# Optimization experiments

Hardware: AMD Instinct MI355X
Metric: run time of the kernel (lower is better)

The kernel has to match this reference:

```python
import jax, jax.numpy as jnp
import numpy as np

G1, G2, G3 = 4.0, 5.0, 10.0   # cfg.SMOOTH.GAMMA1/2/3 (DAMSM defaults)
T_MOCO = 0.05
EPS = 1e-8


def _ce(logits, labels):
    # mean cross-entropy, labels are int class indices
    lp = jax.nn.log_softmax(logits, axis=-1)
    return -jnp.mean(jnp.take_along_axis(lp, labels[:, None], axis=1)[:, 0])


def _norm(x):
    return jnp.sqrt(jnp.sum(x * x, axis=-1, keepdims=True))


def setup_inputs() -> dict:
    key = jax.random.key(0)
    ks = jax.random.split(key, 8)
    B, T, NEF, H, K = 64, 32, 256, 17, 16384
    return {
        "cnn_code": jax.random.normal(ks[0], (B, NEF), jnp.float32),
        "rnn_code": jax.random.normal(ks[1], (B, NEF), jnp.float32),
        "img_features": jax.random.normal(ks[2], (B, NEF, H, H), jnp.float32),
        "words_emb": jax.random.normal(ks[3], (B, T, NEF), jnp.float32),
        "cnn_code_aug": jax.random.normal(ks[4], (B, NEF), jnp.float32),
        "rnn_code_aug": jax.random.normal(ks[5], (B, NEF), jnp.float32),
        "queue": jax.random.normal(ks[6], (NEF, K), jnp.float32),
        "queue_im": jax.random.normal(ks[7], (NEF, K), jnp.float32),
        "sentence_mask": jnp.ones((B, T), jnp.int32),
        "labels": jnp.arange(B, dtype=jnp.int32),
    }


def reference(cnn_code, rnn_code, img_features, words_emb, cnn_code_aug,
              rnn_code_aug, queue, queue_im, sentence_mask, labels):
    B = words_emb.shape[0]
    # ---------- local word-region attention loss (vectorized over the
    # per-sample python loop; sentence_mask is all-ones -> full length) ----------
    q = jnp.transpose(words_emb, (0, 2, 1))                   # [B, nef, T]
    ctx = img_features.reshape(B, img_features.shape[1], -1)  # [B, nef, S]
    # func_attention: scores[i,j,s,t] between query sample i and image j
    scores = jnp.einsum('jcs,ict->ijst', ctx, q)
    attn = jax.nn.softmax(scores, axis=3)        # softmax over words (queryL)
    attn = jax.nn.softmax(G1 * attn, axis=2)     # softmax over regions (sourceL)
    wC = jnp.einsum('jcs,ijst->ijct', ctx, attn)  # weighted context [i,j,nef,T]
    num = jnp.einsum('ict,ijct->ijt', q, wC)
    qn = jnp.sqrt(jnp.sum(q * q, axis=1))[:, None, :]         # [B,1,T]
    wn = jnp.sqrt(jnp.sum(wC * wC, axis=2))                   # [B,B,T]
    cos = num / jnp.clip(qn * wn, EPS, None)                  # [i,j,T]
    sim = jax.nn.logsumexp(G2 * cos, axis=2)                  # log(sum exp(G2*cos))
    S = sim.T * G3                                            # [j, i] as in original cat(dim=1)
    w_loss0 = _ce(S, labels)
    w_loss1 = _ce(S.T, labels)
    # ---------- global contrastive loss ----------
    cn = cnn_code / jnp.clip(_norm(cnn_code), EPS, None)
    rn = rnn_code / jnp.clip(_norm(rnn_code), EPS, None)
    can = cnn_code_aug / jnp.clip(_norm(cnn_code_aug), EPS, None)
    ran = rnn_code_aug / jnp.clip(_norm(rnn_code_aug), EPS, None)
    qz = jax.lax.stop_gradient(queue)
    qzi = jax.lax.stop_gradient(queue_im)
    zeros = jnp.zeros((B,), dtype=labels.dtype)
    log_it = jnp.concatenate([jnp.sum(cn * ran, -1, keepdims=True), cn @ qz], -1) / T_MOCO
    log_ti = jnp.concatenate([jnp.sum(rn * can, -1, keepdims=True), rn @ qzi], -1) / T_MOCO
    m_loss = (_ce(log_it, zeros) + _ce(log_ti, zeros)) / 2.0
    s0 = G3 * (cn @ rn.T)    # cosine(cnn, rnn) * GAMMA3
    s2 = G3 * (rn @ ran.T)   # cosine(rnn, rnn_aug) * GAMMA3
    loss0 = _ce(s0, labels)
    loss1 = _ce(s0.T, labels)
    loss2 = _ce(s2, labels)
    loss3 = _ce(s2.T, labels)
    return jnp.stack([w_loss0, w_loss1, loss0, loss1, m_loss, loss2, loss3])
```

## Files before the change

kernel.cpp:

```cpp
#include <hip/hip_runtime.h>
#include <hip/hip_bf16.h>
#include <math.h>

#define BB   64
#define TT   32
#define CC   256
#define KK   16384
#define G1c  4.0f
#define G2c  5.0f
#define G3c  10.0f
#define INV_T 20.0f
#define EPSF 1e-8f

#define WS_SIM 0
#define WS_S0  4096
#define WS_S2  8192
#define WS_CN  12288
#define WS_RN  28672
#define WS_CAN 45056
#define WS_RAN 61440
#define WS_QN  77824
#define WS_PM  79872
#define WS_PS  (WS_PM + 16384)
#define WS_CNT  (WS_PS + 16384)
#define WS_RNT  (WS_CNT + 16384)
#define WS_CANT (WS_RNT + 16384)
#define WS_RANT (WS_CANT + 16384)
#define WS_F32_TOTAL (WS_RANT + 16384)

#define CTXT_ELEMS (64*320*256)
#define WQ_ELEMS   (64*32*256)
#define WQ_OFF     CTXT_ELEMS
#define CNRN_OFF   (CTXT_ELEMS + WQ_ELEMS)

#define SC_STR 260

typedef __attribute__((ext_vector_type(8))) short short8;
typedef __attribute__((ext_vector_type(4))) short short4v;
typedef __attribute__((ext_vector_type(4))) float float4v;

__device__ __forceinline__ float4v mfma_bf16(short8 a, short8 b, float4v c) {
    return __builtin_amdgcn_mfma_f32_16x16x32_bf16(a, b, c, 0, 0, 0);
}

__device__ __forceinline__ short f2bf(float f) {
    union { float f; unsigned u; } x; x.f = f;
    unsigned r = x.u + 0x7FFFu + ((x.u >> 16) & 1u);
    return (short)(r >> 16);
}

__device__ __forceinline__ short8 ld8(const short* p) {
    short4v lo = *(const short4v*)p;
    short4v hi = *(const short4v*)(p + 4);
    short8 r = {lo[0],lo[1],lo[2],lo[3],hi[0],hi[1],hi[2],hi[3]};
    return r;
}

__global__ __launch_bounds__(256) void prep_kernel(
    const float* __restrict__ cnn, const float* __restrict__ rnn,
    const float* __restrict__ img, const float* __restrict__ wemb,
    const float* __restrict__ cnnA, const float* __restrict__ rnnA,
    float* __restrict__ W)
{
    int bid = blockIdx.x, tid = threadIdx.x;
    short* B16 = (short*)(W + WS_F32_TOTAL);
    short* ctxT = B16;
    short* wq   = B16 + WQ_OFF;
    short* cnrn = B16 + CNRN_OFF;

    if (bid < 256) {
        int mat = bid >> 6, row = bid & 63;
        const float* src = (mat==0)? cnn : (mat==1)? rnn : (mat==2)? cnnA : rnnA;
        float* dst  = W + ((mat==0)? WS_CN  : (mat==1)? WS_RN  : (mat==2)? WS_CAN  : WS_RAN);
        float* dstT = W + ((mat==0)? WS_CNT : (mat==1)? WS_RNT : (mat==2)? WS_CANT : WS_RANT);
        float v = src[row*256 + tid];
        float ss = v*v;
        for (int o=1;o<64;o<<=1) ss += __shfl_xor(ss,o);
        __shared__ float sc[4];
        if ((tid&63)==0) sc[tid>>6] = ss;
        __syncthreads();
        float tot = sc[0]+sc[1]+sc[2]+sc[3];
        float inv = 1.0f / fmaxf(sqrtf(tot), EPSF);
        float nv = v*inv;
        dst[row*256+tid] = nv;
        dstT[tid*64+row] = nv;
        if (mat < 2) cnrn[(mat*64+row)*256 + tid] = f2bf(nv);
    } else if (bid < 320) {
        int i = bid - 256;
        int t = tid >> 3, k = tid & 7;
        const float* wp = wemb + (i*32 + t)*256 + k*32;
        float ss = 0.f;
        for (int c=0;c<32;c++){ float v = wp[c]; ss += v*v; }
        ss += __shfl_xor(ss,1); ss += __shfl_xor(ss,2); ss += __shfl_xor(ss,4);
        if (k==0) W[WS_QN + i*32 + t] = sqrtf(ss);
    } else if (bid < 1600) {
        int b3 = bid - 320; int j = b3 / 20, mt = b3 % 20, s0 = mt*16;
        __shared__ float tile[16*257];
        for (int idx = tid; idx < 4096; idx += 256) {
            int c = idx >> 4, sl = idx & 15, s = s0 + sl;
            float v = (s < 289) ? img[((size_t)(j*256 + c))*289 + s] : 0.0f;
            tile[sl*257 + c] = v;
        }
        __syncthreads();
        for (int idx = tid; idx < 4096; idx += 256) {
            int orr = idx >> 8, c = idx & 255;
            ctxT[((size_t)(j*320 + s0 + orr))*256 + c] = f2bf(tile[orr*257 + c]);
        }
    } else {
        for (int idx = (bid-1600)*256 + tid; idx < WQ_ELEMS; idx += 64*256) {
            wq[idx] = f2bf(wemb[idx]);
        }
    }
}

__global__ __launch_bounds__(256, 2) void attn_moco_kernel(
    const float* __restrict__ queue, const float* __restrict__ queueIm,
    float* __restrict__ W)
{
    __shared__ short ctx_sc[32*SC_STR];
    __shared__ short eTile[2][2][32][36];
    __shared__ float Dp[4][32], Np[4][32];
    __shared__ float wn2P[4][2][2][16];
    __shared__ float redm[4][64], reds[4][64];
    __shared__ float sa0[256], sa1[256];
    __shared__ float part[2][64][4];

    int bid = blockIdx.x, tid = threadIdx.x;
    int lane = tid & 63, wave = tid >> 6;
    int lo16 = lane & 15, quad = lane >> 4;

    const short* B16 = (const short*)(W + WS_F32_TOTAL);

    if (bid >= 320) {
        const short* ctxT = B16;
        const short* wq   = B16 + WQ_OFF;

        int abid = bid - 320;
        int j = abid >> 5, ip = abid & 31;
        int i_l = wave >> 1, mt = wave & 1;
        int i_g = ip*2 + i_l;

        short8 bq[2][8];
        {
            const short* p = wq + i_g*8192;
            #pragma unroll
            for (int nt2=0;nt2<2;nt2++)
                #pragma unroll
                for (int kk=0;kk<8;kk++)
                    bq[nt2][kk] = *(const short8*)(p + (nt2*16+lo16)*256 + kk*32 + quad*8);
        }

        float4v wacc[4][4];
        #pragma unroll
        for (int cm=0;cm<4;cm++)
            #pragma unroll
            for (int cb=0;cb<4;cb++) wacc[cm][cb] = (float4v){0.f,0.f,0.f,0.f};
        float D0=0.f, D1=0.f, N0=0.f, N1=0.f;

        const short* ctxTj = ctxT + (size_t)j * (320*256);
        int s_row = tid >> 3, c0s = (tid & 7)*32;
        int srow_base = mt*16 + quad*4;

        short8 pf[4];
        {
            const short* g = ctxTj + s_row*256 + c0s;
            #pragma unroll
            for (int m=0;m<4;m++) pf[m] = *(const short8*)(g + m*8);
        }

        for (int tile = 0; tile < 10; tile++) {
            {
                short* d = ctx_sc + s_row*SC_STR + c0s;
                #pragma unroll
                for (int k=0;k<8;k++) {
                    short4v w = { pf[k>>1][(k&1)*4+0], pf[k>>1][(k&1)*4+1],
                                  pf[k>>1][(k&1)*4+2], pf[k>>1][(k&1)*4+3] };
                    *(short4v*)(d + k*4) = w;
                }
            }
            __syncthreads();
            if (tile < 9) {
                const short* g = ctxTj + ((tile+1)*32 + s_row)*256 + c0s;
                #pragma unroll
                for (int m=0;m<4;m++) pf[m] = *(const short8*)(g + m*8);
            }

            float4v a0 = {0.f,0.f,0.f,0.f}, a1 = {0.f,0.f,0.f,0.f};
            {
                const short* ar = ctx_sc + (mt*16 + lo16)*SC_STR + quad*8;
                #pragma unroll
                for (int kk=0;kk<8;kk++) {
                    short8 a = ld8(ar + kk*32);
                    a0 = mfma_bf16(a, bq[0][kk], a0);
                    a1 = mfma_bf16(a, bq[1][kk], a1);
                }
            }

            short8 wa[4];
            #pragma unroll
            for (int cm=0;cm<4;cm++) {
                const short* col = ctx_sc + quad*8*SC_STR + wave*64 + cm*16 + lo16;
                short8 v;
                #pragma unroll
                for (int jj=0;jj<8;jj++) v[jj] = col[jj*SC_STR];
                wa[cm] = v;
            }

            int eb = tile & 1;
            #pragma unroll
            for (int r=0;r<4;r++) {
                float mx = fmaxf(a0[r], a1[r]);
                mx = fmaxf(mx, __shfl_xor(mx,1));
                mx = fmaxf(mx, __shfl_xor(mx,2));
                mx = fmaxf(mx, __shfl_xor(mx,4));
                mx = fmaxf(mx, __shfl_xor(mx,8));
                float e0 = __expf(a0[r]-mx), e1 = __expf(a1[r]-mx);
                float z = e0 + e1;
                z += __shfl_xor(z,1); z += __shfl_xor(z,2);
                z += __shfl_xor(z,4); z += __shfl_xor(z,8);
                float rinv = 1.0f/z;
                int s_local = srow_base + r;
                int sg = tile*32 + s_local;
                float ev0 = 0.f, ev1 = 0.f;
                if (sg < 289) {
                    ev0 = __expf(G1c*e0*rinv);
                    ev1 = __expf(G1c*e1*rinv);
                    D0 += ev0; N0 += ev0*a0[r];
                    D1 += ev1; N1 += ev1*a1[r];
                }
                eTile[eb][i_l][lo16][s_local]    = f2bf(ev0);
                eTile[eb][i_l][16+lo16][s_local] = f2bf(ev1);
            }
            __syncthreads();
            {
                short8 bf0 = ld8(&eTile[eb][0][lo16][quad*8]);
                short8 bf1 = ld8(&eTile[eb][0][16+lo16][quad*8]);
                short8 bf2 = ld8(&eTile[eb][1][lo16][quad*8]);
                short8 bf3 = ld8(&eTile[eb][1][16+lo16][quad*8]);
                #pragma unroll
                for (int cm=0;cm<4;cm++) {
                    wacc[cm][0] = mfma_bf16(wa[cm], bf0, wacc[cm][0]);
                    wacc[cm][1] = mfma_bf16(wa[cm], bf1, wacc[cm][1]);
                    wacc[cm][2] = mfma_bf16(wa[cm], bf2, wacc[cm][2]);
                    wacc[cm][3] = mfma_bf16(wa[cm], bf3, wacc[cm][3]);
                }
            }
        }

        D0 += __shfl_xor(D0,16); D0 += __shfl_xor(D0,32);
        D1 += __shfl_xor(D1,16); D1 += __shfl_xor(D1,32);
        N0 += __shfl_xor(N0,16); N0 += __shfl_xor(N0,32);
        N1 += __shfl_xor(N1,16); N1 += __shfl_xor(N1,32);
        if (lane < 16) {
            Dp[wave][lane] = D0; Dp[wave][16+lane] = D1;
            Np[wave][lane] = N0; Np[wave][16+lane] = N1;
        }
        #pragma unroll
        for (int cb=0;cb<4;cb++) {
            float ss = 0.f;
            #pragma unroll
            for (int cm=0;cm<4;cm++)
                #pragma unroll
                for (int r=0;r<4;r++){ float v = wacc[cm][cb][r]; ss += v*v; }
            ss += __shfl_xor(ss,16);
            ss += __shfl_xor(ss,32);
            if (quad==0) wn2P[wave][cb>>1][cb&1][lo16] = ss;
        }
        __syncthreads();

        if (tid < 64) {
            int i_f = tid >> 5, t = tid & 31;
            int nt2 = t >> 4, lo = t & 15;
            float w2 = wn2P[0][i_f][nt2][lo] + wn2P[1][i_f][nt2][lo]
                     + wn2P[2][i_f][nt2][lo] + wn2P[3][i_f][nt2][lo];
            float D = Dp[i_f*2][t] + Dp[i_f*2+1][t];
            float N = Np[i_f*2][t] + Np[i_f*2+1][t];
            int i_gf = ip*2 + i_f;
            float qv = W[WS_QN + i_gf*32 + t];
            float numS = N/D;
            float wnS = sqrtf(w2)/D;
            float v = G2c * (numS / fmaxf(qv*wnS, EPSF));
            float mx = v;
            for (int o=1;o<32;o<<=1) mx = fmaxf(mx, __shfl_xor(mx,o));
            float e = __expf(v-mx);
            for (int o=1;o<32;o<<=1) e += __shfl_xor(e,o);
            if (t==0) W[WS_SIM + i_gf*64 + j] = mx + __logf(e);
        }
    } else if (bid < 256) {
        int mu = bid >> 7, ch = bid & 127;
        const float* Q = mu ? queueIm : queue;
        const short* Abf = B16 + CNRN_OFF + mu*16384;

        short8 afr[4][8];
        #pragma unroll
        for (int mt=0;mt<4;mt++)
            #pragma unroll
            for (int kk=0;kk<8;kk++)
                afr[mt][kk] = *(const short8*)(Abf + (mt*16+lo16)*256 + kk*32 + quad*8);

        float m16[16], s16[16];
        #pragma unroll
        for (int u=0;u<16;u++){ m16[u] = -1e30f; s16[u] = 0.f; }

        for (int t4 = 0; t4 < 2; t4++) {
            int colb = ch*128 + (wave*2 + t4)*16;
            float4v acc[4];
            #pragma unroll
            for (int mt=0;mt<4;mt++) acc[mt] = (float4v){0.f,0.f,0.f,0.f};
            for (int ks = 0; ks < 8; ks++) {
                short8 bfr;
                #pragma unroll
                for (int jj=0;jj<8;jj++) {
                    float bv = Q[(size_t)(ks*32 + quad*8 + jj)*KK + colb + lo16];
                    bfr[jj] = f2bf(bv);
                }
                #pragma unroll
                for (int mt=0;mt<4;mt++) acc[mt] = mfma_bf16(afr[mt][ks], bfr, acc[mt]);
            }
            #pragma unroll
            for (int mt=0;mt<4;mt++)
                #pragma unroll
                for (int r=0;r<4;r++) {
                    float v = acc[mt][r]*INV_T;
                    int u = mt*4+r;
                    float nm = fmaxf(m16[u], v);
                    s16[u] = s16[u]*__expf(m16[u]-nm) + __expf(v-nm);
                    m16[u] = nm;
                }
        }
        #pragma unroll
        for (int u=0;u<16;u++) {
            #pragma unroll
            for (int o=1;o<16;o<<=1) {
                float om = __shfl_xor(m16[u],o), os = __shfl_xor(s16[u],o);
                float nm = fmaxf(m16[u],om);
                s16[u] = s16[u]*__expf(m16[u]-nm) + os*__expf(om-nm);
                m16[u] = nm;
            }
        }
        if (lo16 == 0) {
            #pragma unroll
            for (int u=0;u<16;u++) {
                int row = (u>>2)*16 + quad*4 + (u&3);
                redm[wave][row] = m16[u]; reds[wave][row] = s16[u];
            }
        }
        __syncthreads();
        if (tid < 64) {
            float m = redm[0][tid], s = reds[0][tid];
            for (int w=1;w<4;w++) {
                float om = redm[w][tid], os = reds[w][tid];
                float nm = fmaxf(m,om);
                s = s*__expf(m-nm) + os*__expf(om-nm);
                m = nm;
            }
            W[WS_PM + mu*8192 + ch*64 + tid] = m;
            W[WS_PS + mu*8192 + ch*64 + tid] = s;
        }
    } else {
        int i = bid - 256;
        sa0[tid] = W[WS_CN + i*256 + tid];
        sa1[tid] = W[WS_RN + i*256 + tid];
        __syncthreads();
        const float* B0 = W + WS_RN;
        const float* B1v = W + WS_RAN;
        float av0 = sa0[tid], av1 = sa1[tid];
        for (int jj = 0; jj < 64; jj++) {
            float v0 = av0 * B0[jj*256 + tid];
            float v1 = av1 * B1v[jj*256 + tid];
            for (int o=1;o<64;o<<=1){ v0 += __shfl_xor(v0,o); v1 += __shfl_xor(v1,o); }
            if (lane==0){ part[0][jj][wave]=v0; part[1][jj][wave]=v1; }
        }
        __syncthreads();
        if (tid < 128) {
            int mat = tid>>6, jj = tid&63;
            float s = part[mat][jj][0]+part[mat][jj][1]+part[mat][jj][2]+part[mat][jj][3];
            W[(mat? WS_S2 : WS_S0) + i*64 + jj] = G3c * s;
        }
    }
}

__global__ __launch_bounds__(256) void final_kernel(
    const int* __restrict__ labels, float* __restrict__ W, float* __restrict__ out)
{
    int tid = threadIdx.x;
    __shared__ float mats[3][64][65];
    __shared__ float mmL[2][4][64], ssL[2][4][64];
    __shared__ float cearr[6][64];
    __shared__ float cemoco[128];

    for (int idx = tid; idx < 3*4096; idx += 256) {
        int t = idx >> 12, rem = idx & 4095;
        const float* src = W + (t==0 ? WS_SIM : (t==1 ? WS_S0 : WS_S2));
        mats[t][rem>>6][rem&63] = src[rem];
    }

    {
        int g = tid >> 6, r = tid & 63;
        for (int mu=0; mu<2; mu++) {
            float m = -1e30f, s = 0.f;
            for (int k=0; k<32; k++) {
                int ch = g*32 + k;
                float om = W[WS_PM + mu*8192 + ch*64 + r];
                float os = W[WS_PS + mu*8192 + ch*64 + r];
                float nm = fmaxf(m, om);
                s = s*__expf(m-nm) + os*__expf(om-nm);
                m = nm;
            }
            mmL[mu][g][r] = m; ssL[mu][g][r] = s;
        }
    }
    __syncthreads();

    if (tid < 128) {
        int mu = tid>>6, r = tid&63;
        float m = mmL[mu][0][r], s = ssL[mu][0][r];
        for (int g=1; g<4; g++) {
            float om = mmL[mu][g][r], os = ssL[mu][g][r];
            float nm = fmaxf(m, om);
            s = s*__expf(m-nm) + os*__expf(om-nm);
            m = nm;
        }
        const float* AT = W + (mu ? WS_RNT : WS_CNT);
        const float* BT = W + (mu ? WS_CANT : WS_RANT);
        float dot = 0.f;
        for (int c=0; c<256; c++) dot += AT[c*64 + r]*BT[c*64 + r];
        float v0 = dot*INV_T;
        float nm = fmaxf(m, v0);
        float S = s*__expf(m-nm) + __expf(v0-nm);
        cemoco[tid] = nm + __logf(S) - v0;
    }

    for (int pass=0; pass<2; pass++) {
        int cfg = pass*4 + (tid>>6);
        int row = tid&63;
        if (cfg < 6) {
            int mi; float scale; int colMajor;
            if (cfg==0){ mi=0; scale=G3c; colMajor=1; }
            else if (cfg==1){ mi=0; scale=G3c; colMajor=0; }
            else if (cfg==2){ mi=1; scale=1.f; colMajor=0; }
            else if (cfg==3){ mi=1; scale=1.f; colMajor=1; }
            else if (cfg==4){ mi=2; scale=1.f; colMajor=0; }
            else            { mi=2; scale=1.f; colMajor=1; }
            float mx = -1e30f;
            for (int x=0;x<64;x++) {
                float v = (colMajor? mats[mi][x][row] : mats[mi][row][x])*scale;
                mx = fmaxf(mx, v);
            }
            float se = 0.f;
            for (int x=0;x<64;x++) {
                float v = (colMajor? mats[mi][x][row] : mats[mi][row][x])*scale;
                se += __expf(v-mx);
            }
            int lbl = labels[row];
            float diag = (colMajor? mats[mi][lbl][row] : mats[mi][row][lbl])*scale;
            cearr[cfg][row] = mx + __logf(se) - diag;
        }
    }
    __syncthreads();

    if (tid < 7) {
        float r;
        if (tid == 4) {
            float s0=0.f, s1=0.f;
            for (int k=0;k<64;k++){ s0 += cemoco[k]; s1 += cemoco[64+k]; }
            r = (s0/64.f + s1/64.f)*0.5f;
        } else {
            int cfg = (tid < 4) ? tid : tid - 1;
            float s = 0.f;
            for (int k=0;k<64;k++) s += cearr[cfg][k];
            r = s/64.f;
        }
        out[tid] = r;
    }
}

extern "C" void kernel_launch(void* const* d_in, const int* in_sizes, int n_in,
                              void* d_out, int out_size, void* d_ws, size_t ws_size,
                              hipStream_t stream)
{
    const float* cnn   = (const float*)d_in[0];
    const float* rnn   = (const float*)d_in[1];
    const float* img   = (const float*)d_in[2];
    const float* wemb  = (const float*)d_in[3];
    const float* cnnA  = (const float*)d_in[4];
    const float* rnnA  = (const float*)d_in[5];
    const float* queue   = (const float*)d_in[6];
    const float* queueIm = (const float*)d_in[7];
    const int*   labels  = (const int*)d_in[9];
    float* W   = (float*)d_ws;
    float* out = (float*)d_out;

    prep_kernel<<<1664, 256, 0, stream>>>(cnn, rnn, img, wemb, cnnA, rnnA, W);
    attn_moco_kernel<<<2368, 256, 0, stream>>>(queue, queueIm, W);
    final_kernel<<<1, 256, 0, stream>>>(labels, W, out);
}
```

Before: 250.3 us.

## Swizzle ctx tiles in global memory and use LDS transpose reads

The prep kernel now writes the transposed bf16 image context in a pre-swizzled 32x256 tile layout, so the attention kernel can copy each tile to shared memory with contiguous 16-byte stores and no padding. Score MFMAs swap operand roles so the softmax over words runs along the accumulator rows, which cuts the shuffle reductions. The weighted-context A operand is now fetched with ds_read_b64_tr_b16 transpose loads instead of scalar strided LDS reads. This is meant to remove LDS bank conflicts and scalar shared-memory traffic, at the cost of tricky swizzle index arithmetic and inline asm tied to gfx950.

```diff
diff --git a/kernel.cpp b/kernel.cpp
--- a/kernel.cpp
+++ b/kernel.cpp
@@ -33,8 +33,6 @@
 #define WQ_OFF     CTXT_ELEMS
 #define CNRN_OFF   (CTXT_ELEMS + WQ_ELEMS)
 
-#define SC_STR 260
-
 typedef __attribute__((ext_vector_type(8))) short short8;
 typedef __attribute__((ext_vector_type(4))) short short4v;
 typedef __attribute__((ext_vector_type(4))) float float4v;
@@ -49,11 +47,8 @@
     return (short)(r >> 16);
 }
 
-__device__ __forceinline__ short8 ld8(const short* p) {
-    short4v lo = *(const short4v*)p;
-    short4v hi = *(const short4v*)(p + 4);
-    short8 r = {lo[0],lo[1],lo[2],lo[3],hi[0],hi[1],hi[2],hi[3]};
-    return r;
+__device__ __forceinline__ int swz13(int L) {
+    return L ^ (((L>>10)&3)<<4) ^ ((((L>>6)&1) ^ ((L>>10)&1))<<3);
 }
 
 __global__ __launch_bounds__(256) void prep_kernel(
@@ -94,17 +89,23 @@
         ss += __shfl_xor(ss,1); ss += __shfl_xor(ss,2); ss += __shfl_xor(ss,4);
         if (k==0) W[WS_QN + i*32 + t] = sqrtf(ss);
     } else if (bid < 1600) {
-        int b3 = bid - 320; int j = b3 / 20, mt = b3 % 20, s0 = mt*16;
-        __shared__ float tile[16*257];
+        int b3 = bid - 320; int j = b3 / 20, mt20 = b3 % 20;
+        int half = mt20 & 1;
+        int s0 = mt20 * 16;
+        __shared__ float tbuf[16*257];
         for (int idx = tid; idx < 4096; idx += 256) {
             int c = idx >> 4, sl = idx & 15, s = s0 + sl;
             float v = (s < 289) ? img[((size_t)(j*256 + c))*289 + s] : 0.0f;
-            tile[sl*257 + c] = v;
+            tbuf[sl*257 + c] = v;
         }
         __syncthreads();
+        short* dst = ctxT + (size_t)j*81920 + (size_t)mt20*4096;
         for (int idx = tid; idx < 4096; idx += 256) {
-            int orr = idx >> 8, c = idx & 255;
-            ctxT[((size_t)(j*320 + s0 + orr))*256 + c] = f2bf(tile[orr*257 + c]);
+            int v = half*4096 + idx;
+            int L = swz13(v);
+            int sl = ((L>>10)&3)*4 + ((L>>4)&3);
+            int c  = ((L>>6)&15)*16 + (L&15);
+            dst[idx] = f2bf(tbuf[sl*257 + c]);
         }
     } else {
         for (int idx = (bid-1600)*256 + tid; idx < WQ_ELEMS; idx += 64*256) {
@@ -117,8 +118,8 @@
     const float* __restrict__ queue, const float* __restrict__ queueIm,
     float* __restrict__ W)
 {
-    __shared__ short ctx_sc[32*SC_STR];
-    __shared__ short eTile[2][2][32][36];
+    __shared__ __align__(16) short ctx_sc[8192];
+    __shared__ __align__(16) short eTile[2][2][32][40];
     __shared__ float Dp[4][32], Np[4][32];
     __shared__ float wn2P[4][2][2][16];
     __shared__ float redm[4][64], reds[4][64];
@@ -155,105 +156,116 @@
         for (int cm=0;cm<4;cm++)
             #pragma unroll
             for (int cb=0;cb<4;cb++) wacc[cm][cb] = (float4v){0.f,0.f,0.f,0.f};
-        float D0=0.f, D1=0.f, N0=0.f, N1=0.f;
-
-        const short* ctxTj = ctxT + (size_t)j * (320*256);
-        int s_row = tid >> 3, c0s = (tid & 7)*32;
-        int srow_base = mt*16 + quad*4;
+        float D8[8], N8[8];
+        #pragma unroll
+        for (int u=0;u<8;u++){ D8[u]=0.f; N8[u]=0.f; }
+
+        const short* ctxTj = ctxT + (size_t)j * 81920;
+
+        int s4p = lo16 >> 2;
+        int qh = quad >> 1, ql = quad & 1;
+        int Lb = (mt*4 + s4p)*1024 + qh*64
+               + (((lo16&3) ^ s4p) << 4)
+               + ((ql ^ qh ^ (s4p&1)) << 3);
+        const short* score_base = ctx_sc + Lb;
+        int pcol = mt*16 + (lo16 & 12) + ((lo16 & 3) ^ s4p);
+        unsigned trA = (unsigned)(unsigned long long)(const void*)(&ctx_sc[0])
+                     + (unsigned)(quad*4096 + wave*512 + lo16*2);
+        unsigned trB = trA ^ 16u;
 
         short8 pf[4];
-        {
-            const short* g = ctxTj + s_row*256 + c0s;
-            #pragma unroll
-            for (int m=0;m<4;m++) pf[m] = *(const short8*)(g + m*8);
-        }
+        #pragma unroll
+        for (int m=0;m<4;m++) pf[m] = *(const short8*)(ctxTj + tid*32 + m*8);
+        short8* buf8 = (short8*)ctx_sc;
 
         for (int tile = 0; tile < 10; tile++) {
-            {
-                short* d = ctx_sc + s_row*SC_STR + c0s;
-                #pragma unroll
-                for (int k=0;k<8;k++) {
-                    short4v w = { pf[k>>1][(k&1)*4+0], pf[k>>1][(k&1)*4+1],
-                                  pf[k>>1][(k&1)*4+2], pf[k>>1][(k&1)*4+3] };
-                    *(short4v*)(d + k*4) = w;
-                }
-            }
+            #pragma unroll
+            for (int m=0;m<4;m++) buf8[tid*4+m] = pf[m];
             __syncthreads();
             if (tile < 9) {
-                const short* g = ctxTj + ((tile+1)*32 + s_row)*256 + c0s;
+                const short* g = ctxTj + (tile+1)*8192 + tid*32;
                 #pragma unroll
                 for (int m=0;m<4;m++) pf[m] = *(const short8*)(g + m*8);
             }
 
             float4v a0 = {0.f,0.f,0.f,0.f}, a1 = {0.f,0.f,0.f,0.f};
+            #pragma unroll
+            for (int kk=0;kk<8;kk++) {
+                short8 cf = *(const short8*)(score_base + kk*128);
+                a0 = mfma_bf16(bq[0][kk], cf, a0);
+                a1 = mfma_bf16(bq[1][kk], cf, a1);
+            }
+
+            short4v w00,w01,w10,w11,w20,w21,w30,w31;
+            asm volatile("ds_read_b64_tr_b16 %0, %1 offset:0"    : "=v"(w00) : "v"(trA));
+            asm volatile("ds_read_b64_tr_b16 %0, %1 offset:2048" : "=v"(w01) : "v"(trB));
+            asm volatile("ds_read_b64_tr_b16 %0, %1 offset:128"  : "=v"(w10) : "v"(trB));
+            asm volatile("ds_read_b64_tr_b16 %0, %1 offset:2176" : "=v"(w11) : "v"(trA));
+            asm volatile("ds_read_b64_tr_b16 %0, %1 offset:256"  : "=v"(w20) : "v"(trA));
+            asm volatile("ds_read_b64_tr_b16 %0, %1 offset:2304" : "=v"(w21) : "v"(trB));
+            asm volatile("ds_read_b64_tr_b16 %0, %1 offset:384"  : "=v"(w30) : "v"(trB));
+            asm volatile("ds_read_b64_tr_b16 %0, %1 offset:2432" : "=v"(w31) : "v"(trA));
+
+            float mx = fmaxf(fmaxf(fmaxf(a0[0],a0[1]), fmaxf(a0[2],a0[3])),
+                             fmaxf(fmaxf(a1[0],a1[1]), fmaxf(a1[2],a1[3])));
+            mx = fmaxf(mx, __shfl_xor(mx,16));
+            mx = fmaxf(mx, __shfl_xor(mx,32));
+            float e0[4], e1[4]; float z = 0.f;
+            #pragma unroll
+            for (int r=0;r<4;r++) {
+                e0[r] = __expf(a0[r]-mx); e1[r] = __expf(a1[r]-mx);
+                z += e0[r] + e1[r];
+            }
+            z += __shfl_xor(z,16); z += __shfl_xor(z,32);
+            float grinv = G1c / z;
+            int sg = tile*32 + mt*16 + lo16;
+            int eb = tile & 1;
+            short* et = &eTile[eb][i_l][0][0];
+            #pragma unroll
+            for (int r=0;r<4;r++) {
+                float ev0 = __expf(e0[r]*grinv);
+                float ev1 = __expf(e1[r]*grinv);
+                if (sg < 289) {
+                    D8[r]   += ev0; N8[r]   += ev0*a0[r];
+                    D8[4+r] += ev1; N8[4+r] += ev1*a1[r];
+                }
+                et[(quad*4+r)*40 + pcol]    = f2bf(ev0);
+                et[(16+quad*4+r)*40 + pcol] = f2bf(ev1);
+            }
+            __syncthreads();
+            __builtin_amdgcn_sched_barrier(0);
+
+            short8 wa_[4];
+            wa_[0] = (short8){w00[0],w00[1],w00[2],w00[3], w01[0],w01[1],w01[2],w01[3]};
+            wa_[1] = (short8){w10[0],w10[1],w10[2],w10[3], w11[0],w11[1],w11[2],w11[3]};
+            wa_[2] = (short8){w20[0],w20[1],w20[2],w20[3], w21[0],w21[1],w21[2],w21[3]};
+            wa_[3] = (short8){w30[0],w30[1],w30[2],w30[3], w31[0],w31[1],w31[2],w31[3]};
             {
-                const short* ar = ctx_sc + (mt*16 + lo16)*SC_STR + quad*8;
-                #pragma unroll
-                for (int kk=0;kk<8;kk++) {
-                    short8 a = ld8(ar + kk*32);
-                    a0 = mfma_bf16(a, bq[0][kk], a0);
-                    a1 = mfma_bf16(a, bq[1][kk], a1);
+                const short8 bf00 = *(const short8*)&eTile[eb][0][lo16][quad*8];
+                const short8 bf01 = *(const short8*)&eTile[eb][0][16+lo16][quad*8];
+                const short8 bf10 = *(const short8*)&eTile[eb][1][lo16][quad*8];
+                const short8 bf11 = *(const short8*)&eTile[eb][1][16+lo16][quad*8];
+                #pragma unroll
+                for (int cm=0;cm<4;cm++) {
+                    wacc[cm][0] = mfma_bf16(wa_[cm], bf00, wacc[cm][0]);
+                    wacc[cm][1] = mfma_bf16(wa_[cm], bf01, wacc[cm][1]);
+                    wacc[cm][2] = mfma_bf16(wa_[cm], bf10, wacc[cm][2]);
+                    wacc[cm][3] = mfma_bf16(wa_[cm], bf11, wacc[cm][3]);
                 }
             }
-
-            short8 wa[4];
-            #pragma unroll
-            for (int cm=0;cm<4;cm++) {
-                const short* col = ctx_sc + quad*8*SC_STR + wave*64 + cm*16 + lo16;
-                short8 v;
-                #pragma unroll
-                for (int jj=0;jj<8;jj++) v[jj] = col[jj*SC_STR];
-                wa[cm] = v;
-            }
-
-            int eb = tile & 1;
-            #pragma unroll
-            for (int r=0;r<4;r++) {
-                float mx = fmaxf(a0[r], a1[r]);
-                mx = fmaxf(mx, __shfl_xor(mx,1));
-                mx = fmaxf(mx, __shfl_xor(mx,2));
-                mx = fmaxf(mx, __shfl_xor(mx,4));
-                mx = fmaxf(mx, __shfl_xor(mx,8));
-                float e0 = __expf(a0[r]-mx), e1 = __expf(a1[r]-mx);
-                float z = e0 + e1;
-                z += __shfl_xor(z,1); z += __shfl_xor(z,2);
-                z += __shfl_xor(z,4); z += __shfl_xor(z,8);
-                float rinv = 1.0f/z;
-                int s_local = srow_base + r;
-                int sg = tile*32 + s_local;
-                float ev0 = 0.f, ev1 = 0.f;
-                if (sg < 289) {
-                    ev0 = __expf(G1c*e0*rinv);
-                    ev1 = __expf(G1c*e1*rinv);
-                    D0 += ev0; N0 += ev0*a0[r];
-                    D1 += ev1; N1 += ev1*a1[r];
-                }
-                eTile[eb][i_l][lo16][s_local]    = f2bf(ev0);
-                eTile[eb][i_l][16+lo16][s_local] = f2bf(ev1);
-            }
-            __syncthreads();
-            {
-                short8 bf0 = ld8(&eTile[eb][0][lo16][quad*8]);
-                short8 bf1 = ld8(&eTile[eb][0][16+lo16][quad*8]);
-                short8 bf2 = ld8(&eTile[eb][1][lo16][quad*8]);
-                short8 bf3 = ld8(&eTile[eb][1][16+lo16][quad*8]);
-                #pragma unroll
-                for (int cm=0;cm<4;cm++) {
-                    wacc[cm][0] = mfma_bf16(wa[cm], bf0, wacc[cm][0]);
-                    wacc[cm][1] = mfma_bf16(wa[cm], bf1, wacc[cm][1]);
-                    wacc[cm][2] = mfma_bf16(wa[cm], bf2, wacc[cm][2]);
-                    wacc[cm][3] = mfma_bf16(wa[cm], bf3, wacc[cm][3]);
-                }
-            }
-        }
-
-        D0 += __shfl_xor(D0,16); D0 += __shfl_xor(D0,32);
-        D1 += __shfl_xor(D1,16); D1 += __shfl_xor(D1,32);
-        N0 += __shfl_xor(N0,16); N0 += __shfl_xor(N0,32);
-        N1 += __shfl_xor(N1,16); N1 += __shfl_xor(N1,32);
-        if (lane < 16) {
-            Dp[wave][lane] = D0; Dp[wave][16+lane] = D1;
-            Np[wave][lane] = N0; Np[wave][16+lane] = N1;
+        }
+
+        #pragma unroll
+        for (int u=0;u<8;u++) {
+            float d = D8[u], n = N8[u];
+            d += __shfl_xor(d,1); d += __shfl_xor(d,2);
+            d += __shfl_xor(d,4); d += __shfl_xor(d,8);
+            n += __shfl_xor(n,1); n += __shfl_xor(n,2);
+            n += __shfl_xor(n,4); n += __shfl_xor(n,8);
+            if (lo16 == 0) {
+                int t = (u>>2)*16 + quad*4 + (u&3);
+                Dp[wave][t] = d; Np[wave][t] = n;
+            }
         }
         #pragma unroll
         for (int cb=0;cb<4;cb++) {
```

New measurement: 233.1 us. -6.9%, faster.
